# Performance work log

Hardware: AMD Instinct MI355X
Metric: run time of the kernel (lower is better)

The kernel has to match this reference:

```python
import jax
import jax.numpy as jnp
from jax import lax
import numpy as np

BLANK = 0  # blank label index (init_kwargs)
B, T, U1, V = 8, 128, 65, 1024  # U1 = max_target_len + 1
U = U1 - 1


def setup_inputs() -> dict:
    key = jax.random.key(0)
    k1, k2, k3, k4 = jax.random.split(key, 4)
    logits = jax.random.normal(k1, (B, T, U1, V), dtype=jnp.float32)
    logit_lens = jax.random.randint(k2, (B,), T // 2, T + 1, dtype=jnp.int32)
    # labels cannot be the blank index -> sample from [1, V)
    y = jax.random.randint(k3, (B, U), 1, V, dtype=jnp.int32)
    y_lens = jax.random.randint(k4, (B,), U // 2, U + 1, dtype=jnp.int32)
    return {"logits": logits, "logit_lens": logit_lens, "y": y, "y_lens": y_lens}


def _rnnt_loss(logits, y, logit_lens, y_lens):
    # logits: [B, T, U+1, V]; y: [B, U] int; lengths: [B] int
    logp = jax.nn.log_softmax(logits.astype(jnp.float32), axis=-1)
    lp_blank = logp[..., BLANK]  # [B, T, U+1]
    # label emission logprob at (t, u): logp[b, t, u, y[b, u]] for u < U
    yb = jnp.broadcast_to(y[:, None, :, None].astype(jnp.int32), (B, T, U, 1))
    lp_label = jnp.take_along_axis(logp[:, :, :U, :], yb, axis=3)[..., 0]  # [B, T, U]

    # alpha trellis: alpha[t, u] = logaddexp(alpha[t-1,u] + blank[t-1,u],
    #                                        alpha[t,u-1] + label[t,u-1])
    # init row t = 0: pure label path
    a0 = jnp.concatenate(
        [jnp.zeros((B, 1), jnp.float32), jnp.cumsum(lp_label[:, 0, :], axis=1)], axis=1
    )  # [B, U+1]

    def t_step(prev, inp):
        blank_prev, label_t = inp  # [B, U+1], [B, U]
        c = prev + blank_prev  # vertical (time) transition contribution
        a_first = c[:, 0]  # u = 0: only blank path

        def u_step(carry, xs):
            c_u, l_prev = xs  # each [B]
            a = jnp.logaddexp(c_u, carry + l_prev)
            return a, a

        _, rest = lax.scan(u_step, a_first, (c[:, 1:].T, label_t.T))  # [U, B]
        a = jnp.concatenate([a_first[:, None], rest.T], axis=1)  # [B, U+1]
        return a, a

    _, alphas_rest = lax.scan(
        t_step, a0,
        (jnp.transpose(lp_blank[:, :-1], (1, 0, 2)), jnp.transpose(lp_label[:, 1:], (1, 0, 2))),
    )  # [T-1, B, U+1]
    alphas = jnp.concatenate([a0[None], alphas_rest], axis=0)  # [T, B, U+1]
    alphas = jnp.transpose(alphas, (1, 0, 2))  # [B, T, U+1]

    b_idx = jnp.arange(B)
    t_end = logit_lens.astype(jnp.int32) - 1
    u_end = y_lens.astype(jnp.int32)
    log_like = alphas[b_idx, t_end, u_end] + lp_blank[b_idx, t_end, u_end]
    losses = -log_like  # [B]
    return jnp.mean(losses)  # reduction='mean' over batch


def reference(logits, logit_lens, y, y_lens):
    return _rnnt_loss(logits, y, logit_lens, y_lens)
```

## Files before the change

kernel.cpp:

```cpp
#include <hip/hip_runtime.h>
#include <math.h>

#define BB 8
#define TT 128
#define U1 65
#define UU 64
#define VV 1024
#define DSTR 66
#define NDIAG 208
#define NEGINF -1e30f
#define LOG2E 1.4426950408889634f
#define LN2   0.6931471805599453f

__device__ __forceinline__ float shfl_up1(float x) {
  return __int_as_float(__builtin_amdgcn_update_dpp(
      0, __float_as_int(x), 0x138, 0xf, 0xf, false));
}

#define ROWSUM(x0, x1, x2, x3, e00, ss)                                  \
  e00 = __builtin_amdgcn_exp2f((x0).x * LOG2E);                          \
  ss  = e00                                                              \
      + __builtin_amdgcn_exp2f((x0).y * LOG2E)                           \
      + __builtin_amdgcn_exp2f((x0).z * LOG2E)                           \
      + __builtin_amdgcn_exp2f((x0).w * LOG2E)                           \
      + __builtin_amdgcn_exp2f((x1).x * LOG2E)                           \
      + __builtin_amdgcn_exp2f((x1).y * LOG2E)                           \
      + __builtin_amdgcn_exp2f((x1).z * LOG2E)                           \
      + __builtin_amdgcn_exp2f((x1).w * LOG2E)                           \
      + __builtin_amdgcn_exp2f((x2).x * LOG2E)                           \
      + __builtin_amdgcn_exp2f((x2).y * LOG2E)                           \
      + __builtin_amdgcn_exp2f((x2).z * LOG2E)                           \
      + __builtin_amdgcn_exp2f((x2).w * LOG2E)                           \
      + __builtin_amdgcn_exp2f((x3).x * LOG2E)                           \
      + __builtin_amdgcn_exp2f((x3).y * LOG2E)                           \
      + __builtin_amdgcn_exp2f((x3).z * LOG2E)                           \
      + __builtin_amdgcn_exp2f((x3).w * LOG2E);

__global__ __launch_bounds__(256) void lse_gather(
    const float* __restrict__ logits, const int* __restrict__ y,
    const int* __restrict__ logit_lens, const int* __restrict__ y_lens,
    float* __restrict__ comb) {
  const int wave = threadIdx.x >> 6;
  const int lane = threadIdx.x & 63;
  const int rowA = blockIdx.x * 8 + wave * 2;
  const int rowB = rowA + 1;
  const int b    = rowA / (TT * U1);
  const int tlen = logit_lens[b];
  const int ulen = y_lens[b];
  float* cb = comb + (size_t)b * NDIAG * DSTR * 2;

  const int uA = rowA % U1, tA = (rowA / U1) % TT;
  const int uB = rowB % U1, tB = (rowB / U1) % TT;

  if (lane == 0) {
    if (tA == 0) cb[2 * (uA * DSTR + uA) + 0]   = 0.f;
    if (uA == 0) cb[2 * ((tA + 1) * DSTR) + 1]  = 0.f;
    if (tB == 0) cb[2 * (uB * DSTR + uB) + 0]   = 0.f;
    if (uB == 0) cb[2 * ((tB + 1) * DSTR) + 1]  = 0.f;
  }

  const bool actA = (tA < tlen) && (uA <= ulen);
  const bool actB = (tB < tlen) && (uB <= ulen);
  if (!actA && !actB) return;

  const float4* rpA = (const float4*)(logits + (size_t)rowA * VV);
  const float4* rpB = (const float4*)(logits + (size_t)rowB * VV);
  float4 a0, a1, a2, a3, b0, b1, b2, b3;
  if (actA) { a0 = rpA[lane];       a1 = rpA[lane + 64];
              a2 = rpA[lane + 128]; a3 = rpA[lane + 192]; }
  if (actB) { b0 = rpB[lane];       b1 = rpB[lane + 64];
              b2 = rpB[lane + 128]; b3 = rpB[lane + 192]; }

  float labA = 0.f, labB = 0.f;
  if (lane == 0) {
    if (actA && uA < UU) labA = logits[(size_t)rowA * VV + y[b * UU + uA]];
    if (actB && uB < UU) labB = logits[(size_t)rowB * VV + y[b * UU + uB]];
  }

  if (actA) {
    float e00, ss;
    ROWSUM(a0, a1, a2, a3, e00, ss)
#pragma unroll
    for (int s = 32; s >= 1; s >>= 1) ss += __shfl_xor(ss, s);
    if (lane == 0) {
      const float rss = __builtin_amdgcn_rcpf(ss);
      const int dd = tA + uA + 1;
      cb[2 * (dd * DSTR + uA) + 0] = e00 * rss;
      if (uA < UU)
        cb[2 * (dd * DSTR + uA + 1) + 1] =
            __builtin_amdgcn_exp2f(labA * LOG2E) * rss;
    }
  }
  if (actB) {
    float e00, ss;
    ROWSUM(b0, b1, b2, b3, e00, ss)
#pragma unroll
    for (int s = 32; s >= 1; s >>= 1) ss += __shfl_xor(ss, s);
    if (lane == 0) {
      const float rss = __builtin_amdgcn_rcpf(ss);
      const int dd = tB + uB + 1;
      cb[2 * (dd * DSTR + uB) + 0] = e00 * rss;
      if (uB < UU)
        cb[2 * (dd * DSTR + uB + 1) + 1] =
            __builtin_amdgcn_exp2f(labB * LOG2E) * rss;
    }
  }
}

__global__ __launch_bounds__(256) void alpha_dp(
    const float2* __restrict__ comb, const int* __restrict__ logit_lens,
    const int* __restrict__ y_lens, float* __restrict__ losses) {
  const int b   = blockIdx.x;
  const int tid = threadIdx.x;

  const int tEnd = logit_lens[b] - 1;
  const int uEnd = y_lens[b];
  const int dT   = tEnd + uEnd;
  const int uclamp = (uEnd < 63) ? uEnd : 63;

  __shared__ __align__(16) float2 cs[NDIAG * DSTR];
  {
    const int npairs2 = ((dT + 10) * DSTR) / 2;
    const float4* g = (const float4*)(comb + (size_t)b * NDIAG * DSTR);
    float4* s4 = (float4*)cs;
    for (int i = tid; i < npairs2; i += 256) s4[i] = g[i];
  }
  __syncthreads();
  if (tid >= 64) return;
  const int lane = tid;

  const float2* cp = cs + lane;
  const float2* ce = cs + 64;

  float V    = (lane == 0) ? 1.f : 0.f;
  float V64  = 0.f;
  int   Rexp = 0;

#define STEP(cc, ee)                                      \
  {                                                       \
    const float Vl  = shfl_up1(V);                        \
    const float t64 = V * (ee).y;       \
    V   = V * (cc).x + Vl * (cc).y;                       \
    V64 = V64 * (ee).x + t64;                             \
  }

#define RESCALE(dd)                                                     \
  {                                                                     \
    const int ref = min(max((dd) - (tEnd >> 1), 0), uclamp);            \
    const float vr = __int_as_float(                                    \
        __builtin_amdgcn_readlane(__float_as_int(V), ref));             \
    const int eb = (__float_as_int(vr) >> 23) & 0xff;                   \
    if (eb > 0 && eb < 255) {                                           \
      const float sc = __int_as_float((254 - eb) << 23);   \
      V *= sc; V64 *= sc; Rexp += eb - 127;                             \
    }                                                                   \
  }

  float2 c0 = cp[66 * 1], c1 = cp[66 * 2], c2 = cp[66 * 3], c3 = cp[66 * 4],
         c4 = cp[66 * 5], c5 = cp[66 * 6], c6 = cp[66 * 7], c7 = cp[66 * 8];
  float2 e0 = ce[66 * 1], e1_ = ce[66 * 2], e2_ = ce[66 * 3], e3_ = ce[66 * 4],
         e4_ = ce[66 * 5], e5_ = ce[66 * 6], e6_ = ce[66 * 7], e7_ = ce[66 * 8];

  int d = 1;
  for (; d + 7 <= dT; d += 8) {
    const float2 n0 = cp[66 * (d + 8)],  n1 = cp[66 * (d + 9)];
    const float2 n2 = cp[66 * (d + 10)], n3 = cp[66 * (d + 11)];
    const float2 n4 = cp[66 * (d + 12)], n5 = cp[66 * (d + 13)];
    const float2 n6 = cp[66 * (d + 14)], n7 = cp[66 * (d + 15)];
    const float2 f0 = ce[66 * (d + 8)],  f1 = ce[66 * (d + 9)];
    const float2 f2 = ce[66 * (d + 10)], f3 = ce[66 * (d + 11)];
    const float2 f4 = ce[66 * (d + 12)], f5 = ce[66 * (d + 13)];
    const float2 f6 = ce[66 * (d + 14)], f7 = ce[66 * (d + 15)];
    STEP(c0, e0)  STEP(c1, e1_) STEP(c2, e2_) STEP(c3, e3_)
    RESCALE(d + 3)
    STEP(c4, e4_) STEP(c5, e5_) STEP(c6, e6_) STEP(c7, e7_)
    RESCALE(d + 7)
    c0 = n0; c1 = n1; c2 = n2; c3 = n3; c4 = n4; c5 = n5; c6 = n6; c7 = n7;
    e0 = f0; e1_ = f1; e2_ = f2; e3_ = f3; e4_ = f4; e5_ = f5; e6_ = f6; e7_ = f7;
  }
  if (d <= dT) { STEP(c0, e0)  RESCALE(d) ++d; }
  if (d <= dT) { STEP(c1, e1_) RESCALE(d) ++d; }
  if (d <= dT) { STEP(c2, e2_) RESCALE(d) ++d; }
  if (d <= dT) { STEP(c3, e3_) RESCALE(d) ++d; }
  if (d <= dT) { STEP(c4, e4_) RESCALE(d) ++d; }
  if (d <= dT) { STEP(c5, e5_) RESCALE(d) ++d; }
  if (d <= dT) { STEP(c6, e6_) RESCALE(d) ++d; }
#undef STEP
#undef RESCALE

  const float Vres = (uEnd == 64) ? V64 : V;
  const int  sel   = (uEnd == 64) ? 63 : uEnd;
  if (lane == sel) {
    const float a = (float)Rexp + __builtin_amdgcn_logf(Vres)
                  + __builtin_amdgcn_logf(cs[(dT + 1) * DSTR + uEnd].x);
    losses[b] = -a * LN2;
  }
}

__global__ void finalize(const float* __restrict__ losses, float* __restrict__ out) {
  if (threadIdx.x == 0) {
    float s = 0.f;
#pragma unroll
    for (int i = 0; i < BB; ++i) s += losses[i];
    out[0] = s * (1.f / BB);
  }
}

extern "C" void kernel_launch(void* const* d_in, const int* in_sizes, int n_in,
                              void* d_out, int out_size, void* d_ws, size_t ws_size,
                              hipStream_t stream) {
  const float* logits     = (const float*)d_in[0];
  const int*   logit_lens = (const int*)d_in[1];
  const int*   y          = (const int*)d_in[2];
  const int*   y_lens     = (const int*)d_in[3];
  float* out = (float*)d_out;

  float2* comb   = (float2*)d_ws;
  float*  losses = (float*)(comb + (size_t)BB * NDIAG * DSTR);

  const int rows = BB * TT * U1;
  lse_gather<<<rows / 8, 256, 0, stream>>>(logits, y, logit_lens, y_lens, (float*)comb);
  alpha_dp<<<BB, 256, 0, stream>>>(comb, logit_lens, y_lens, losses);
  finalize<<<1, 64, 0, stream>>>(losses, out);
}
```

Before: 47.65 us.

## Process 8-timestep strips per wave with double-buffered row loads

```diff
diff --git a/kernel.cpp b/kernel.cpp
--- a/kernel.cpp
+++ b/kernel.cpp
@@ -42,68 +42,71 @@
     float* __restrict__ comb) {
   const int wave = threadIdx.x >> 6;
   const int lane = threadIdx.x & 63;
-  const int rowA = blockIdx.x * 8 + wave * 2;
-  const int rowB = rowA + 1;
-  const int b    = rowA / (TT * U1);
-  const int tlen = logit_lens[b];
-  const int ulen = y_lens[b];
+  const int s  = blockIdx.x * 4 + wave;
+  const int b  = s / 1040;
+  const int sp = s % 1040;
+  const int u  = sp % U1;
+  const int t0 = (sp / U1) * 8;
+
   float* cb = comb + (size_t)b * NDIAG * DSTR * 2;
 
-  const int uA = rowA % U1, tA = (rowA / U1) % TT;
-  const int uB = rowB % U1, tB = (rowB / U1) % TT;
-
   if (lane == 0) {
-    if (tA == 0) cb[2 * (uA * DSTR + uA) + 0]   = 0.f;
-    if (uA == 0) cb[2 * ((tA + 1) * DSTR) + 1]  = 0.f;
-    if (tB == 0) cb[2 * (uB * DSTR + uB) + 0]   = 0.f;
-    if (uB == 0) cb[2 * ((tB + 1) * DSTR) + 1]  = 0.f;
-  }
-
-  const bool actA = (tA < tlen) && (uA <= ulen);
-  const bool actB = (tB < tlen) && (uB <= ulen);
-  if (!actA && !actB) return;
-
-  const float4* rpA = (const float4*)(logits + (size_t)rowA * VV);
-  const float4* rpB = (const float4*)(logits + (size_t)rowB * VV);
-  float4 a0, a1, a2, a3, b0, b1, b2, b3;
-  if (actA) { a0 = rpA[lane];       a1 = rpA[lane + 64];
-              a2 = rpA[lane + 128]; a3 = rpA[lane + 192]; }
-  if (actB) { b0 = rpB[lane];       b1 = rpB[lane + 64];
-              b2 = rpB[lane + 128]; b3 = rpB[lane + 192]; }
-
-  float labA = 0.f, labB = 0.f;
-  if (lane == 0) {
-    if (actA && uA < UU) labA = logits[(size_t)rowA * VV + y[b * UU + uA]];
-    if (actB && uB < UU) labB = logits[(size_t)rowB * VV + y[b * UU + uB]];
-  }
-
-  if (actA) {
+    if (t0 == 0) cb[2 * (u * DSTR + u) + 0] = 0.f;
+    if (u == 0) {
+#pragma unroll
+      for (int j = 0; j < 8; ++j)
+        cb[2 * ((t0 + j + 1) * DSTR) + 1] = 0.f;
+    }
+  }
+
+  const int tl = logit_lens[b];
+  const int ul = y_lens[b];
+  const int k  = (u <= ul) ? min(max(tl - t0, 0), 8) : 0;
+  if (k == 0) return;
+
+  const bool havel = (u < UU);
+  const int  yidx  = havel ? y[b * UU + u] : 0;
+  const size_t rbase = ((size_t)b * (TT * U1) + (size_t)t0 * U1 + u) * VV;
+
+  auto issue = [&](float4& X0, float4& X1, float4& X2, float4& X3,
+                   float& lab, int j) {
+    const float* rj = logits + rbase + (size_t)j * U1 * VV;
+    const float4* p_ = (const float4*)rj;
+    X0 = p_[lane]; X1 = p_[lane + 64]; X2 = p_[lane + 128]; X3 = p_[lane + 192];
+    if (lane == 0 && havel) lab = rj[yidx];
+  };
+
+  auto reduce_store = [&](const float4& X0, const float4& X1,
+                          const float4& X2, const float4& X3,
+                          float lab, int j) {
     float e00, ss;
-    ROWSUM(a0, a1, a2, a3, e00, ss)
+    ROWSUM(X0, X1, X2, X3, e00, ss)
 #pragma unroll
-    for (int s = 32; s >= 1; s >>= 1) ss += __shfl_xor(ss, s);
+    for (int sh = 32; sh >= 1; sh >>= 1) ss += __shfl_xor(ss, sh);
     if (lane == 0) {
       const float rss = __builtin_amdgcn_rcpf(ss);
-      const int dd = tA + uA + 1;
-      cb[2 * (dd * DSTR + uA) + 0] = e00 * rss;
-      if (uA < UU)
-        cb[2 * (dd * DSTR + uA + 1) + 1] =
-            __builtin_amdgcn_exp2f(labA * LOG2E) * rss;
+      const int dd = t0 + j + u + 1;
+      cb[2 * (dd * DSTR + u) + 0] = e00 * rss;
+      if (havel)
+        cb[2 * (dd * DSTR + u + 1) + 1] =
+            __builtin_amdgcn_exp2f(lab * LOG2E) * rss;
     }
-  }
-  if (actB) {
-    float e00, ss;
-    ROWSUM(b0, b1, b2, b3, e00, ss)
-#pragma unroll
-    for (int s = 32; s >= 1; s >>= 1) ss += __shfl_xor(ss, s);
-    if (lane == 0) {
-      const float rss = __builtin_amdgcn_rcpf(ss);
-      const int dd = tB + uB + 1;
-      cb[2 * (dd * DSTR + uB) + 0] = e00 * rss;
-      if (uB < UU)
-        cb[2 * (dd * DSTR + uB + 1) + 1] =
-            __builtin_amdgcn_exp2f(labB * LOG2E) * rss;
-    }
+  };
+
+  float4 A0, A1, A2, A3, B0, B1, B2, B3;
+  float labA = 0.f, labB = 0.f;
+
+  issue(A0, A1, A2, A3, labA, 0);
+  if (k > 1) issue(B0, B1, B2, B3, labB, 1);
+
+  int j = 0;
+  while (true) {
+    reduce_store(A0, A1, A2, A3, labA, j);
+    if (j + 2 < k) issue(A0, A1, A2, A3, labA, j + 2);
+    ++j; if (j >= k) break;
+    reduce_store(B0, B1, B2, B3, labB, j);
+    if (j + 2 < k) issue(B0, B1, B2, B3, labB, j + 2);
+    ++j; if (j >= k) break;
   }
 }
 
@@ -218,8 +221,9 @@
   float2* comb   = (float2*)d_ws;
   float*  losses = (float*)(comb + (size_t)BB * NDIAG * DSTR);
 
-  const int rows = BB * TT * U1;
-  lse_gather<<<rows / 8, 256, 0, stream>>>(logits, y, logit_lens, y_lens, (float*)comb);
+  const int nstrips = BB * (TT / 8) * U1;
+  lse_gather<<<nstrips / 4, 256, 0, stream>>>(logits, y, logit_lens, y_lens,
+                                              (float*)comb);
   alpha_dp<<<BB, 256, 0, stream>>>(comb, logit_lens, y_lens, losses);
   finalize<<<1, 64, 0, stream>>>(losses, out);
 }
```

Result: no change. 47.54 us (-0.2%).
